# Performance work log

Hardware: AMD Instinct MI355X
Metric: run time of the kernel (lower is better)

The kernel has to match this reference:

```python
import jax, jax.numpy as jnp
import numpy as np

NEG_SLOPE = 0.2  # PyG GATConv default negative_slope
EPS = 1e-16


def gat_conv(x, src, dst, num_nodes, W, att_src, att_dst, bias, concat):
    """PyG-style GATConv (eval mode, no dropout). att_*: [H, C]."""
    H, C = att_src.shape
    h = (x @ W).reshape(num_nodes, H, C)                      # [N,H,C]
    a_s = jnp.einsum('nhc,hc->nh', h, att_src)                # [N,H]
    a_d = jnp.einsum('nhc,hc->nh', h, att_dst)                # [N,H]
    e = jax.nn.leaky_relu(a_s[src] + a_d[dst], NEG_SLOPE)     # [E,H]
    # segment softmax over edges grouped by destination node
    m = jax.lax.stop_gradient(jax.ops.segment_max(e, dst, num_segments=num_nodes))
    ex = jnp.exp(e - m[dst])
    denom = jax.ops.segment_sum(ex, dst, num_segments=num_nodes)
    alpha = ex / (denom[dst] + EPS)                           # [E,H]
    msg = h[src] * alpha[:, :, None]                          # [E,H,C]
    out = jax.ops.segment_sum(msg, dst, num_segments=num_nodes)  # [N,H,C]
    out = out.reshape(num_nodes, H * C) if concat else out.mean(axis=1)
    return out + bias


def setup_inputs() -> dict:
    key = jax.random.key(0)
    ks = jax.random.split(key, 12)
    N, E = 65536, 1310720
    IN, HID, OUT, HEADS = 768, 128, 2, 8
    C1 = HID // HEADS  # 16
    s = 0.05
    return {
        'x': jax.random.normal(ks[0], (N, IN), jnp.float32),
        'edge_index': jax.random.randint(ks[1], (2, E), 0, N, jnp.int64),
        'W1': jax.random.normal(ks[2], (IN, HEADS * C1), jnp.float32) * s,
        'att_src1': jax.random.normal(ks[3], (HEADS, C1), jnp.float32) * s,
        'att_dst1': jax.random.normal(ks[4], (HEADS, C1), jnp.float32) * s,
        'b1': jnp.zeros((HID,), jnp.float32),
        'Wp': jax.random.normal(ks[5], (IN, HID), jnp.float32) * s,
        'bp': jnp.zeros((HID,), jnp.float32),
        'W2': jax.random.normal(ks[6], (HID, OUT), jnp.float32) * s,
        'att_src2': jax.random.normal(ks[7], (1, OUT), jnp.float32) * s,
        'att_dst2': jax.random.normal(ks[8], (1, OUT), jnp.float32) * s,
        'b2': jnp.zeros((OUT,), jnp.float32),
    }


def reference(x, edge_index, W1, att_src1, att_dst1, b1, Wp, bp, W2, att_src2, att_dst2, b2):
    N = x.shape[0]
    loops = jnp.arange(N, dtype=edge_index.dtype)  # add_self_loops=True
    src = jnp.concatenate([edge_index[0], loops])
    dst = jnp.concatenate([edge_index[1], loops])
    # eval mode: dropout is identity
    h1 = gat_conv(x, src, dst, N, W1, att_src1, att_dst1, b1, concat=True)
    h = jax.nn.elu(h1 + x @ Wp + bp)  # residual projection + ELU
    return gat_conv(h, src, dst, N, W2, att_src2, att_dst2, b2, concat=False)
```

## Files before the change

### kernel.cpp

```cpp
#include <hip/hip_runtime.h>
#include <hip/hip_bf16.h>
#include <math.h>

#define NEG_SLOPE 0.2f

typedef __attribute__((ext_vector_type(8))) short short8;
typedef __attribute__((ext_vector_type(4))) float float4v;

__device__ __forceinline__ unsigned f2bf(float f) {
  unsigned u = __builtin_bit_cast(unsigned, f);
  return (u + 0x7fffu + ((u >> 16) & 1u)) >> 16;
}
__device__ __forceinline__ float bflo(unsigned u) {
  return __builtin_bit_cast(float, u << 16);
}
__device__ __forceinline__ float bfhi(unsigned u) {
  return __builtin_bit_cast(float, u & 0xffff0000u);
}
__device__ __forceinline__ unsigned cvtpk(float lo, float hi) {
  unsigned r;
  asm("v_cvt_pk_bf16_f32 %0, %1, %2" : "=v"(r) : "v"(lo), "v"(hi));
  return r;
}
__device__ __forceinline__ void gl2lds16(const void* g, void* l) {
  __builtin_amdgcn_global_load_lds(
      (const __attribute__((address_space(1))) unsigned*)g,
      (__attribute__((address_space(3))) unsigned*)l, 16, 0, 0);
}

__global__ __launch_bounds__(256) void convert_w(const float* __restrict__ W1,
                                                 const float* __restrict__ Wp,
                                                 short* __restrict__ Wt) {
  int k = blockIdx.x;
  int c = threadIdx.x;
  float v = (c < 128) ? W1[k * 128 + c] : Wp[k * 128 + (c - 128)];
  Wt[(size_t)c * 768 + k] = (short)f2bf(v);
}

__global__ __launch_bounds__(256) void gemm_mfma(const float* __restrict__ x,
                                                 const short* __restrict__ Wt,
                                                 float* __restrict__ proj,
                                                 unsigned* __restrict__ h1bf) {
  __shared__ float As[2][2048];
  __shared__ short Bs[2][8192];
  const int tid = threadIdx.x;
  const int w = tid >> 6, l = tid & 63;
  const int l15 = l & 15, l4 = l >> 4;
  const int row0 = blockIdx.x * 64;

  const char* ag[2];
#pragma unroll
  for (int i = 0; i < 2; i++) {
    int row = w * 16 + i * 8 + (l >> 3);
    int q = (l & 7) ^ (l >> 3);
    ag[i] = (const char*)x + (size_t)(row0 + row) * 3072 + q * 16;
  }
  const char* bg[4];
#pragma unroll
  for (int i = 0; i < 4; i++) {
    int c = w * 64 + i * 16 + (l >> 2);
    int q = (l & 3) ^ ((l >> 3) & 3);
    bg[i] = (const char*)Wt + (size_t)c * 1536 + q * 16;
  }

  float4v acc[4][4] = {};
  const int pc = l4 ^ ((l15 >> 1) & 3);
  const int p0 = (l4 * 2) ^ (l15 & 7);

  auto stage = [&](int b, int t) {
    gl2lds16(ag[0] + t * 128, (char*)As[b] + w * 2048 + 0 * 1024);
    gl2lds16(ag[1] + t * 128, (char*)As[b] + w * 2048 + 1 * 1024);
    gl2lds16(bg[0] + t * 64, (char*)Bs[b] + w * 4096 + 0 * 1024);
    gl2lds16(bg[1] + t * 64, (char*)Bs[b] + w * 4096 + 1 * 1024);
    gl2lds16(bg[2] + t * 64, (char*)Bs[b] + w * 4096 + 2 * 1024);
    gl2lds16(bg[3] + t * 64, (char*)Bs[b] + w * 4096 + 3 * 1024);
  };
  auto compute = [&](int b) {
    const char* asb = (const char*)As[b];
    const char* bsb = (const char*)Bs[b];
    short8 afr[4];
#pragma unroll
    for (int rt = 0; rt < 4; rt++) {
      const int r = rt * 16 + l15;
      float4 lo = *(const float4*)(asb + r * 128 + p0 * 16);
      float4 hi = *(const float4*)(asb + r * 128 + (p0 ^ 1) * 16);
      uint4 pk;
      pk.x = cvtpk(lo.x, lo.y);
      pk.y = cvtpk(lo.z, lo.w);
      pk.z = cvtpk(hi.x, hi.y);
      pk.w = cvtpk(hi.z, hi.w);
      afr[rt] = __builtin_bit_cast(short8, pk);
    }
#pragma unroll
    for (int ct = 0; ct < 4; ct++) {
      const int c = w * 64 + ct * 16 + l15;
      short8 bfr = *(const short8*)(bsb + c * 64 + pc * 16);
#pragma unroll
      for (int rt = 0; rt < 4; rt++)
        acc[rt][ct] =
            __builtin_amdgcn_mfma_f32_16x16x32_bf16(afr[rt], bfr, acc[rt][ct], 0, 0, 0);
    }
  };

  stage(0, 0);
  __syncthreads();
  for (int t = 0; t < 24; t += 2) {
    stage(1, t + 1);
    compute(0);
    __syncthreads();
    if (t + 2 < 24) stage(0, t + 2);
    compute(1);
    __syncthreads();
  }

  const int colbase = w * 64;
  if (w < 2) {
#pragma unroll
    for (int ct = 0; ct < 4; ct++) {
      const int c = colbase + ct * 16 + l15;
#pragma unroll
      for (int rt = 0; rt < 4; rt++) {
#pragma unroll
        for (int r = 0; r < 4; r++) {
          const int R = row0 + rt * 16 + l4 * 4 + r;
          unsigned u = f2bf(acc[rt][ct][r]);
          unsigned up = __shfl_xor(u, 1);
          if ((l15 & 1) == 0) h1bf[(size_t)R * 64 + (c >> 1)] = u | (up << 16);
        }
      }
    }
  } else {
#pragma unroll
    for (int ct = 0; ct < 4; ct++) {
      const int c = colbase - 128 + ct * 16 + l15;
#pragma unroll
      for (int rt = 0; rt < 4; rt++) {
#pragma unroll
        for (int r = 0; r < 4; r++) {
          const int R = row0 + rt * 16 + l4 * 4 + r;
          proj[(size_t)R * 128 + c] = acc[rt][ct][r];
        }
      }
    }
  }
}

__global__ __launch_bounds__(256) void attn1b(const uint4* __restrict__ h1bf4,
                                              const float* __restrict__ att_src1,
                                              const float* __restrict__ att_dst1,
                                              float* __restrict__ a_s1,
                                              float* __restrict__ a_d1) {
  const int t = blockIdx.x * 256 + threadIdx.x;
  const int n = t >> 3, h = t & 7;
  uint4 q0 = h1bf4[(size_t)n * 16 + h * 2];
  uint4 q1 = h1bf4[(size_t)n * 16 + h * 2 + 1];
  float v[16];
  v[0] = bflo(q0.x); v[1] = bfhi(q0.x); v[2] = bflo(q0.y); v[3] = bfhi(q0.y);
  v[4] = bflo(q0.z); v[5] = bfhi(q0.z); v[6] = bflo(q0.w); v[7] = bfhi(q0.w);
  v[8] = bflo(q1.x); v[9] = bfhi(q1.x); v[10] = bflo(q1.y); v[11] = bfhi(q1.y);
  v[12] = bflo(q1.z); v[13] = bfhi(q1.z); v[14] = bflo(q1.w); v[15] = bfhi(q1.w);
  float as = 0.f, ad = 0.f;
#pragma unroll
  for (int i = 0; i < 16; i++) {
    as += v[i] * att_src1[h * 16 + i];
    ad += v[i] * att_dst1[h * 16 + i];
  }
  a_s1[t] = as;
  a_d1[t] = ad;
}

__global__ void init_counts(int* counts, int N) {
  int i = blockIdx.x * blockDim.x + threadIdx.x;
  if (i < N) counts[i] = 1;
}

__global__ void hist_kernel(const int* __restrict__ dst, int* counts,
                            int* __restrict__ rank, int E) {
  int i = blockIdx.x * blockDim.x + threadIdx.x;
  int base = i * 4;
  if (base + 3 < E) {
    int4 d = *(const int4*)&dst[base];
    int4 r;
    r.x = atomicAdd(&counts[d.x], 1);
    r.y = atomicAdd(&counts[d.y], 1);
    r.z = atomicAdd(&counts[d.z], 1);
    r.w = atomicAdd(&counts[d.w], 1);
    *(int4*)&rank[base] = r;
  } else {
    for (int j = base; j < E; j++) rank[j] = atomicAdd(&counts[dst[j]], 1);
  }
}

__global__ __launch_bounds__(256) void scan_a(const int* __restrict__ counts,
                                              int* offsets, int* bsum) {
  __shared__ int s[256];
  int t = threadIdx.x, idx = blockIdx.x * 256 + t;
  int v = counts[idx];
  s[t] = v;
  __syncthreads();
  for (int d = 1; d < 256; d <<= 1) {
    int x = (t >= d) ? s[t - d] : 0;
    __syncthreads();
    s[t] += x;
    __syncthreads();
  }
  offsets[idx] = s[t] - v;
  if (t == 255) bsum[blockIdx.x] = s[t];
}

__global__ __launch_bounds__(256) void scan_b(int* bsum) {
  __shared__ int s[256];
  int t = threadIdx.x;
  int v = bsum[t];
  s[t] = v;
  __syncthreads();
  for (int d = 1; d < 256; d <<= 1) {
    int x = (t >= d) ? s[t - d] : 0;
    __syncthreads();
    s[t] += x;
    __syncthreads();
  }
  bsum[t] = s[t] - v;
}

__global__ __launch_bounds__(256) void scan_c(int* offsets, const int* bsum,
                                              int* sortedsrc, int N, int Etot) {
  int t = threadIdx.x, idx = blockIdx.x * 256 + t;
  int off = offsets[idx] + bsum[blockIdx.x];
  offsets[idx] = off;
  sortedsrc[off] = idx;
  if (idx == 0) offsets[N] = Etot;
}

__global__ void scatter_edges(const int* __restrict__ src,
                              const int* __restrict__ dst,
                              const int* __restrict__ rank,
                              const int* __restrict__ offsets,
                              int* __restrict__ sortedsrc, int E) {
  int i = blockIdx.x * blockDim.x + threadIdx.x;
  int base = i * 4;
  if (base + 3 < E) {
    int4 s = *(const int4*)&src[base];
    int4 d = *(const int4*)&dst[base];
    int4 r = *(const int4*)&rank[base];
    sortedsrc[offsets[d.x] + r.x] = s.x;
    sortedsrc[offsets[d.y] + r.y] = s.y;
    sortedsrc[offsets[d.z] + r.z] = s.z;
    sortedsrc[offsets[d.w] + r.w] = s.w;
  } else {
    for (int j = base; j < E; j++)
      sortedsrc[offsets[dst[j]] + rank[j]] = src[j];
  }
}

__global__ __launch_bounds__(256) void agg1_fused(
    const uint4* __restrict__ h1bf4, const float* __restrict__ proj,
    const float* __restrict__ a_s1, const float* __restrict__ a_d1,
    const int* __restrict__ offsets, const int* __restrict__ sortedsrc,
    const float* __restrict__ b1, const float* __restrict__ bp,
    const float* __restrict__ W2, const float* __restrict__ att_s2,
    const float* __restrict__ att_d2, float* __restrict__ h2,
    float* __restrict__ as2, float* __restrict__ ad2) {
  const int t = threadIdx.x;
  const int n = blockIdx.x * 16 + (t >> 4);
  const int k = t & 15;
  const int hd = k >> 1;
  const float ad = a_d1[n * 8 + hd];
  const int begin = offsets[n], end = offsets[n + 1];
  float acc[8] = {};
  float aw = 0.f;
  int j = begin;
  for (; j + 4 <= end; j += 4) {
    int s0 = sortedsrc[j], s1 = sortedsrc[j + 1];
    int s2 = sortedsrc[j + 2], s3 = sortedsrc[j + 3];
    float e0 = a_s1[s0 * 8 + hd], e1 = a_s1[s1 * 8 + hd];
    float e2 = a_s1[s2 * 8 + hd], e3 = a_s1[s3 * 8 + hd];
    uint4 q0 = h1bf4[(size_t)s0 * 16 + k];
    uint4 q1 = h1bf4[(size_t)s1 * 16 + k];
    uint4 q2 = h1bf4[(size_t)s2 * 16 + k];
    uint4 q3 = h1bf4[(size_t)s3 * 16 + k];
    e0 += ad; e1 += ad; e2 += ad; e3 += ad;
    float w0 = __expf(e0 > 0.f ? e0 : NEG_SLOPE * e0);
    float w1 = __expf(e1 > 0.f ? e1 : NEG_SLOPE * e1);
    float w2 = __expf(e2 > 0.f ? e2 : NEG_SLOPE * e2);
    float w3 = __expf(e3 > 0.f ? e3 : NEG_SLOPE * e3);
    acc[0] += w0 * bflo(q0.x) + w1 * bflo(q1.x) + w2 * bflo(q2.x) + w3 * bflo(q3.x);
    acc[1] += w0 * bfhi(q0.x) + w1 * bfhi(q1.x) + w2 * bfhi(q2.x) + w3 * bfhi(q3.x);
    acc[2] += w0 * bflo(q0.y) + w1 * bflo(q1.y) + w2 * bflo(q2.y) + w3 * bflo(q3.y);
    acc[3] += w0 * bfhi(q0.y) + w1 * bfhi(q1.y) + w2 * bfhi(q2.y) + w3 * bfhi(q3.y);
    acc[4] += w0 * bflo(q0.z) + w1 * bflo(q1.z) + w2 * bflo(q2.z) + w3 * bflo(q3.z);
    acc[5] += w0 * bfhi(q0.z) + w1 * bfhi(q1.z) + w2 * bfhi(q2.z) + w3 * bfhi(q3.z);
    acc[6] += w0 * bflo(q0.w) + w1 * bflo(q1.w) + w2 * bflo(q2.w) + w3 * bflo(q3.w);
    acc[7] += w0 * bfhi(q0.w) + w1 * bfhi(q1.w) + w2 * bfhi(q2.w) + w3 * bfhi(q3.w);
    aw += (w0 + w1) + (w2 + w3);
  }
  for (; j < end; j++) {
    int s0 = sortedsrc[j];
    float e0 = a_s1[s0 * 8 + hd] + ad;
    uint4 q0 = h1bf4[(size_t)s0 * 16 + k];
    float w0 = __expf(e0 > 0.f ? e0 : NEG_SLOPE * e0);
    acc[0] += w0 * bflo(q0.x);
    acc[1] += w0 * bfhi(q0.x);
    acc[2] += w0 * bflo(q0.y);
    acc[3] += w0 * bfhi(q0.y);
    acc[4] += w0 * bflo(q0.z);
    acc[5] += w0 * bfhi(q0.z);
    acc[6] += w0 * bflo(q0.w);
    acc[7] += w0 * bfhi(q0.w);
    aw += w0;
  }
  const float inv = 1.f / (aw + 1e-16f);
  const float4 pj0 = *(const float4*)&proj[(size_t)n * 128 + k * 8];
  const float4 pj1 = *(const float4*)&proj[(size_t)n * 128 + k * 8 + 4];
  const float4 b1a = *(const float4*)&b1[k * 8];
  const float4 b1b = *(const float4*)&b1[k * 8 + 4];
  const float4 bpa = *(const float4*)&bp[k * 8];
  const float4 bpb = *(const float4*)&bp[k * 8 + 4];
  float v[8];
  v[0] = acc[0] * inv + pj0.x + b1a.x + bpa.x;
  v[1] = acc[1] * inv + pj0.y + b1a.y + bpa.y;
  v[2] = acc[2] * inv + pj0.z + b1a.z + bpa.z;
  v[3] = acc[3] * inv + pj0.w + b1a.w + bpa.w;
  v[4] = acc[4] * inv + pj1.x + b1b.x + bpb.x;
  v[5] = acc[5] * inv + pj1.y + b1b.y + bpb.y;
  v[6] = acc[6] * inv + pj1.z + b1b.z + bpb.z;
  v[7] = acc[7] * inv + pj1.w + b1b.w + bpb.w;
  float p0 = 0.f, p1 = 0.f;
#pragma unroll
  for (int i = 0; i < 8; i++) {
    float vi = v[i] > 0.f ? v[i] : (__expf(v[i]) - 1.f);
    float2 w2 = *(const float2*)&W2[(k * 8 + i) * 2];
    p0 += vi * w2.x;
    p1 += vi * w2.y;
  }
#pragma unroll
  for (int off = 8; off; off >>= 1) {
    p0 += __shfl_xor(p0, off);
    p1 += __shfl_xor(p1, off);
  }
  if (k == 0) {
    h2[2 * n] = p0;
    h2[2 * n + 1] = p1;
    as2[n] = p0 * att_s2[0] + p1 * att_s2[1];
    ad2[n] = p0 * att_d2[0] + p1 * att_d2[1];
  }
}

__global__ __launch_bounds__(256) void agg2(
    const float* __restrict__ h2, const float* __restrict__ as2,
    const float* __restrict__ ad2, const int* __restrict__ offsets,
    const int* __restrict__ sortedsrc, const float* __restrict__ b2,
    float* __restrict__ out, int N) {
  const int node = blockIdx.x * 16 + (threadIdx.x >> 4);
  const int lane = threadIdx.x & 15;
  const int begin = offsets[node], end = offsets[node + 1];
  const float ad = ad2[node];
  float acc0 = 0.f, acc1 = 0.f, aw = 0.f;
  for (int j = begin + lane; j < end; j += 16) {
    int s = sortedsrc[j];
    float e = as2[s] + ad;
    float w = __expf(e > 0.f ? e : NEG_SLOPE * e);
    float2 hh = *(const float2*)&h2[2 * s];
    acc0 += w * hh.x;
    acc1 += w * hh.y;
    aw += w;
  }
#pragma unroll
  for (int off = 8; off; off >>= 1) {
    acc0 += __shfl_xor(acc0, off);
    acc1 += __shfl_xor(acc1, off);
    aw += __shfl_xor(aw, off);
  }
  if (lane == 0) {
    float inv = 1.f / (aw + 1e-16f);
    out[2 * node] = acc0 * inv + b2[0];
    out[2 * node + 1] = acc1 * inv + b2[1];
  }
}

extern "C" void kernel_launch(void* const* d_in, const int* in_sizes, int n_in,
                              void* d_out, int out_size, void* d_ws,
                              size_t ws_size, hipStream_t stream) {
  const float* x = (const float*)d_in[0];
  const int* edge_index = (const int*)d_in[1];
  const float* W1 = (const float*)d_in[2];
  const float* att_src1 = (const float*)d_in[3];
  const float* att_dst1 = (const float*)d_in[4];
  const float* b1 = (const float*)d_in[5];
  const float* Wp = (const float*)d_in[6];
  const float* bp = (const float*)d_in[7];
  const float* W2 = (const float*)d_in[8];
  const float* att_src2 = (const float*)d_in[9];
  const float* att_dst2 = (const float*)d_in[10];
  const float* b2 = (const float*)d_in[11];
  float* out = (float*)d_out;

  const int N = in_sizes[0] / 768;
  const int E = in_sizes[1] / 2;
  const int Etot = E + N;
  const int* src = edge_index;
  const int* dst = edge_index + E;

  char* ws = (char*)d_ws;
  size_t off = 0;
  auto alloc = [&](size_t bytes) {
    size_t cur = off;
    off += (bytes + 255) & ~(size_t)255;
    return (void*)(ws + cur);
  };
  float* proj = (float*)alloc((size_t)N * 128 * 4);
  unsigned* h1bf = (unsigned*)alloc((size_t)N * 64 * 4);
  float* a_s1 = (float*)alloc((size_t)N * 8 * 4);
  float* a_d1 = (float*)alloc((size_t)N * 8 * 4);
  float* h2 = (float*)alloc((size_t)N * 2 * 4);
  float* as2 = (float*)alloc((size_t)N * 4);
  float* ad2 = (float*)alloc((size_t)N * 4);
  int* counts = (int*)alloc((size_t)N * 4);
  int* offsets = (int*)alloc(((size_t)N + 1) * 4);
  int* rank = (int*)alloc((size_t)E * 4);
  int* bsum = (int*)alloc(256 * 4);
  int* sortedsrc = (int*)alloc((size_t)Etot * 4);
  short* Wt = (short*)alloc((size_t)256 * 768 * 2);

  convert_w<<<768, 256, 0, stream>>>(W1, Wp, Wt);
  gemm_mfma<<<N / 64, 256, 0, stream>>>(x, Wt, proj, h1bf);
  attn1b<<<N * 8 / 256, 256, 0, stream>>>((const uint4*)h1bf, att_src1,
                                          att_dst1, a_s1, a_d1);
  init_counts<<<(N + 255) / 256, 256, 0, stream>>>(counts, N);
  hist_kernel<<<(E / 4 + 255) / 256, 256, 0, stream>>>(dst, counts, rank, E);
  scan_a<<<N / 256, 256, 0, stream>>>(counts, offsets, bsum);
  scan_b<<<1, 256, 0, stream>>>(bsum);
  scan_c<<<N / 256, 256, 0, stream>>>(offsets, bsum, sortedsrc, N, Etot);
  scatter_edges<<<(E / 4 + 255) / 256, 256, 0, stream>>>(src, dst, rank,
                                                         offsets, sortedsrc, E);
  agg1_fused<<<N / 16, 256, 0, stream>>>((const uint4*)h1bf, proj, a_s1, a_d1,
                                         offsets, sortedsrc, b1, bp, W2,
                                         att_src2, att_dst2, h2, as2, ad2);
  agg2<<<N / 16, 256, 0, stream>>>(h2, as2, ad2, offsets, sortedsrc, b2, out,
                                   N);
}
```

Before: 504.6 us.

## Convert A tile to bf16 once on load instead of per-wave in compute

The A operand (x rows) is now loaded through registers, converted to bf16 once per element, and written to LDS in a swizzled bf16 layout, instead of being copied to LDS as fp32 via direct global-to-LDS loads and reconverted by every wave in compute. This halves A's LDS footprint and removes redundant conversions across the four waves. Launch bounds are set to 4 blocks per CU to raise occupancy. The trade-off is that the A path now goes through VGPRs, adding register pressure and load latency that the software pipeline must hide.

```diff
diff --git a/kernel.cpp b/kernel.cpp
--- a/kernel.cpp
+++ b/kernel.cpp
@@ -37,24 +37,20 @@
   Wt[(size_t)c * 768 + k] = (short)f2bf(v);
 }
 
-__global__ __launch_bounds__(256) void gemm_mfma(const float* __restrict__ x,
-                                                 const short* __restrict__ Wt,
-                                                 float* __restrict__ proj,
-                                                 unsigned* __restrict__ h1bf) {
-  __shared__ float As[2][2048];
+__global__ __launch_bounds__(256, 4) void gemm_mfma(
+    const float* __restrict__ x, const short* __restrict__ Wt,
+    float* __restrict__ proj, unsigned* __restrict__ h1bf) {
+  __shared__ short As[2][2048];
   __shared__ short Bs[2][8192];
   const int tid = threadIdx.x;
   const int w = tid >> 6, l = tid & 63;
   const int l15 = l & 15, l4 = l >> 4;
   const int row0 = blockIdx.x * 64;
 
-  const char* ag[2];
-#pragma unroll
-  for (int i = 0; i < 2; i++) {
-    int row = w * 16 + i * 8 + (l >> 3);
-    int q = (l & 7) ^ (l >> 3);
-    ag[i] = (const char*)x + (size_t)(row0 + row) * 3072 + q * 16;
-  }
+  const float* xsrc = x + (size_t)(row0 + (tid >> 2)) * 768 + (tid & 3) * 8;
+  const int awoff = (tid >> 2) * 64 + (((tid & 3) ^ ((tid >> 3) & 3)) << 4);
+  const int aoff = l15 * 64 + ((l4 ^ ((l15 >> 1) & 3)) << 4);
+
   const char* bg[4];
 #pragma unroll
   for (int i = 0; i < 4; i++) {
@@ -62,39 +58,38 @@
     int q = (l & 3) ^ ((l >> 3) & 3);
     bg[i] = (const char*)Wt + (size_t)c * 1536 + q * 16;
   }
+  const int pc = l4 ^ ((l15 >> 1) & 3);
 
   float4v acc[4][4] = {};
-  const int pc = l4 ^ ((l15 >> 1) & 3);
-  const int p0 = (l4 * 2) ^ (l15 & 7);
-
-  auto stage = [&](int b, int t) {
-    gl2lds16(ag[0] + t * 128, (char*)As[b] + w * 2048 + 0 * 1024);
-    gl2lds16(ag[1] + t * 128, (char*)As[b] + w * 2048 + 1 * 1024);
-    gl2lds16(bg[0] + t * 64, (char*)Bs[b] + w * 4096 + 0 * 1024);
-    gl2lds16(bg[1] + t * 64, (char*)Bs[b] + w * 4096 + 1 * 1024);
-    gl2lds16(bg[2] + t * 64, (char*)Bs[b] + w * 4096 + 2 * 1024);
-    gl2lds16(bg[3] + t * 64, (char*)Bs[b] + w * 4096 + 3 * 1024);
+
+  auto loadA = [&](int t, float4& r0, float4& r1) {
+    const float* p = xsrc + t * 32;
+    r0 = *(const float4*)p;
+    r1 = *(const float4*)(p + 4);
   };
-  auto compute = [&](int b) {
-    const char* asb = (const char*)As[b];
-    const char* bsb = (const char*)Bs[b];
+  auto writeA = [&](short* asb, const float4& r0, const float4& r1) {
+    uint4 pk;
+    pk.x = cvtpk(r0.x, r0.y);
+    pk.y = cvtpk(r0.z, r0.w);
+    pk.z = cvtpk(r1.x, r1.y);
+    pk.w = cvtpk(r1.z, r1.w);
+    *(uint4*)((char*)asb + awoff) = pk;
+  };
+  auto stageB = [&](short* bsb, int t) {
+    gl2lds16(bg[0] + t * 64, (char*)bsb + w * 4096 + 0 * 1024);
+    gl2lds16(bg[1] + t * 64, (char*)bsb + w * 4096 + 1 * 1024);
+    gl2lds16(bg[2] + t * 64, (char*)bsb + w * 4096 + 2 * 1024);
+    gl2lds16(bg[3] + t * 64, (char*)bsb + w * 4096 + 3 * 1024);
+  };
+  auto compute = [&](const short* asb, const short* bsb) {
     short8 afr[4];
 #pragma unroll
-    for (int rt = 0; rt < 4; rt++) {
-      const int r = rt * 16 + l15;
-      float4 lo = *(const float4*)(asb + r * 128 + p0 * 16);
-      float4 hi = *(const float4*)(asb + r * 128 + (p0 ^ 1) * 16);
-      uint4 pk;
-      pk.x = cvtpk(lo.x, lo.y);
-      pk.y = cvtpk(lo.z, lo.w);
-      pk.z = cvtpk(hi.x, hi.y);
-      pk.w = cvtpk(hi.z, hi.w);
-      afr[rt] = __builtin_bit_cast(short8, pk);
-    }
+    for (int rt = 0; rt < 4; rt++)
+      afr[rt] = *(const short8*)((const char*)asb + rt * 1024 + aoff);
 #pragma unroll
     for (int ct = 0; ct < 4; ct++) {
-      const int c = w * 64 + ct * 16 + l15;
-      short8 bfr = *(const short8*)(bsb + c * 64 + pc * 16);
+      short8 bfr =
+          *(const short8*)((const char*)bsb + (w * 64 + ct * 16 + l15) * 64 + pc * 16);
 #pragma unroll
       for (int rt = 0; rt < 4; rt++)
         acc[rt][ct] =
@@ -102,14 +97,23 @@
     }
   };
 
-  stage(0, 0);
+  float4 r0, r1;
+  loadA(0, r0, r1);
+  stageB(Bs[0], 0);
+  writeA(As[0], r0, r1);
   __syncthreads();
   for (int t = 0; t < 24; t += 2) {
-    stage(1, t + 1);
-    compute(0);
-    __syncthreads();
-    if (t + 2 < 24) stage(0, t + 2);
-    compute(1);
+    loadA(t + 1, r0, r1);
+    stageB(Bs[1], t + 1);
+    compute(As[0], Bs[0]);
+    writeA(As[1], r0, r1);
+    __syncthreads();
+    if (t + 2 < 24) {
+      loadA(t + 2, r0, r1);
+      stageB(Bs[0], t + 2);
+    }
+    compute(As[1], Bs[1]);
+    if (t + 2 < 24) writeA(As[0], r0, r1);
     __syncthreads();
   }
 
```

Result: no change. 500.9 us (-0.7%).
